# Kernel optimization log

Measured on AMD Instinct MI355X. Metric: run time of the kernel, lower is better.

Reference implementation:

```python
import jax, jax.numpy as jnp
import numpy as np

B, N, D, H, F = 2, 2048, 1024, 16, 4096
E = D // H
EPS = 1e-5

def layer_norm(x, g, b):
    mu = jnp.mean(x, axis=-1, keepdims=True)
    var = jnp.var(x, axis=-1, keepdims=True)
    return (x - mu) * jax.lax.rsqrt(var + EPS) * g + b

def setup_inputs() -> dict:
    key = jax.random.key(0)
    ks = jax.random.split(key, 16)
    s = lambda k, sh, fan: jax.random.normal(k, sh, jnp.float32) * (1.0 / np.sqrt(fan))
    return {
        'x': jax.random.normal(ks[0], (B, N, D), jnp.float32),
        'wq': s(ks[1], (D, D), D), 'bq': jnp.zeros((D,), jnp.float32),
        'wk': s(ks[2], (D, D), D), 'bk': jnp.zeros((D,), jnp.float32),
        'wv': s(ks[3], (D, D), D), 'bv': jnp.zeros((D,), jnp.float32),
        'w1': s(ks[4], (F, D), D), 'b1': jnp.zeros((F,), jnp.float32),
        'ln_mlp_g': jnp.ones((F,), jnp.float32), 'ln_mlp_b': jnp.zeros((F,), jnp.float32),
        'w2': s(ks[5], (D, F), F), 'b2': jnp.zeros((D,), jnp.float32),
        'ln1_g': jnp.ones((D,), jnp.float32), 'ln1_b': jnp.zeros((D,), jnp.float32),
        'ln2_g': jnp.ones((D,), jnp.float32), 'ln2_b': jnp.zeros((D,), jnp.float32),
    }

def reference(x, wq, bq, wk, bk, wv, bv, w1, b1, ln_mlp_g, ln_mlp_b, w2, b2, ln1_g, ln1_b, ln2_g, ln2_b):
    h = layer_norm(x, ln1_g, ln1_b)                       # [B,N,D]
    q = (h @ wq.T + bq).reshape(B, N, H, E).transpose(0, 2, 1, 3)  # [B,H,N,E]
    k = (h @ wk.T + bk).reshape(B, N, H, E).transpose(0, 2, 1, 3)
    v = (h @ wv.T + bv).reshape(B, N, H, E).transpose(0, 2, 1, 3)
    # faithful to source: score = q@k^T / sqrt(1/emb_dim) == q@k^T * sqrt(emb_dim)
    score = jnp.einsum('bhne,bhme->bhnm', q, k) * np.sqrt(D).astype(np.float32)
    causal = jnp.tril(jnp.ones((N, N), bool))
    score = jnp.where(causal[None, None], score, -jnp.inf)
    weight = jax.nn.softmax(score, axis=-1)
    attn = jnp.einsum('bhnm,bhme->bhne', weight, v)       # [B,H,N,E]
    attn = attn.transpose(0, 2, 1, 3).reshape(B, N, D)
    x = x + attn
    h2 = layer_norm(x, ln2_g, ln2_b)
    m = h2 @ w1.T + b1                                    # [B,N,F]
    m = jax.nn.relu(layer_norm(m, ln_mlp_g, ln_mlp_b))
    # faithful: no second residual in the source forward
    return m @ w2.T + b2
```

## Files before the change

### kernel.cpp

```cpp
#include <hip/hip_runtime.h>
#include <cstdint>

typedef __bf16 bf16_t;
typedef bf16_t bf16x8 __attribute__((ext_vector_type(8)));
typedef bf16_t bf16x4 __attribute__((ext_vector_type(4)));
typedef float  floatx4 __attribute__((ext_vector_type(4)));

#define GLD_LDS(g, l) __builtin_amdgcn_global_load_lds( \
    (const __attribute__((address_space(1))) unsigned int*)(g), \
    (__attribute__((address_space(3))) unsigned int*)(l), 16, 0, 0)

#define MFMA_BF16_16x16x32 __builtin_amdgcn_mfma_f32_16x16x32_bf16

__global__ __launch_bounds__(256) void prep(
    const float* __restrict__ wq, const float* __restrict__ wk,
    const float* __restrict__ wv, const float* __restrict__ w1,
    const float* __restrict__ w2, const float* __restrict__ bq,
    const float* __restrict__ bk,
    bf16_t* __restrict__ wqk_hi, bf16_t* __restrict__ wqk_lo,
    bf16_t* __restrict__ wvb, bf16_t* __restrict__ w1b, bf16_t* __restrict__ w2b,
    float* __restrict__ bqk) {
  const int blk = blockIdx.x, tid = threadIdx.x;
  if (blk < 2048) {
    const int qk = blk >> 10;
    const int i  = (blk & 1023) * 256 + tid;
    const float* src = qk ? wk : wq;
    float4 v = ((const float4*)src)[i];
    float f[4] = {v.x, v.y, v.z, v.w};
    bf16x4 h, l;
    #pragma unroll
    for (int j = 0; j < 4; ++j) { h[j] = (bf16_t)f[j]; l[j] = (bf16_t)(f[j] - (float)h[j]); }
    ((bf16x4*)(wqk_hi + qk * 1024 * 1024))[i] = h;
    ((bf16x4*)(wqk_lo + qk * 1024 * 1024))[i] = l;
  } else if (blk < 3072) {
    const int i = (blk - 2048) * 256 + tid;
    float4 v = ((const float4*)wv)[i];
    bf16x4 o; o[0]=(bf16_t)v.x; o[1]=(bf16_t)v.y; o[2]=(bf16_t)v.z; o[3]=(bf16_t)v.w;
    ((bf16x4*)wvb)[i] = o;
  } else if (blk < 7168) {
    const int i = (blk - 3072) * 256 + tid;
    float4 v = ((const float4*)w1)[i];
    bf16x4 o; o[0]=(bf16_t)v.x; o[1]=(bf16_t)v.y; o[2]=(bf16_t)v.z; o[3]=(bf16_t)v.w;
    ((bf16x4*)w1b)[i] = o;
  } else if (blk < 11264) {
    const int i = (blk - 7168) * 256 + tid;
    float4 v = ((const float4*)w2)[i];
    bf16x4 o; o[0]=(bf16_t)v.x; o[1]=(bf16_t)v.y; o[2]=(bf16_t)v.z; o[3]=(bf16_t)v.w;
    ((bf16x4*)w2b)[i] = o;
  } else {
    const int i = (blk - 11264) * 256 + tid;
    if (i < 1024) { bqk[i] = bq[i]; bqk[1024 + i] = bk[i]; }
  }
}


__device__ __forceinline__ void block_sum2(float& s, float& ss, float* red) {
  #pragma unroll
  for (int off = 32; off > 0; off >>= 1) {
    s  += __shfl_down(s, off);
    ss += __shfl_down(ss, off);
  }
  const int wave = threadIdx.x >> 6;
  if ((threadIdx.x & 63) == 0) { red[wave * 2] = s; red[wave * 2 + 1] = ss; }
  __syncthreads();
  s  = red[0] + red[2] + red[4] + red[6];
  ss = red[1] + red[3] + red[5] + red[7];
}

__global__ __launch_bounds__(256) void ln_fwd_split(const float* __restrict__ x,
    const float* __restrict__ g, const float* __restrict__ b,
    bf16_t* __restrict__ out_hi, bf16_t* __restrict__ out_lo) {
  __shared__ float red[8];
  const size_t row = blockIdx.x;
  float4 v = ((const float4*)(x + row * 1024))[threadIdx.x];
  float s  = v.x + v.y + v.z + v.w;
  float ss = v.x*v.x + v.y*v.y + v.z*v.z + v.w*v.w;
  block_sum2(s, ss, red);
  const float mu  = s * (1.f / 1024.f);
  const float var = ss * (1.f / 1024.f) - mu * mu;
  const float rs  = rsqrtf(var + 1e-5f);
  float4 gg = ((const float4*)g)[threadIdx.x];
  float4 bb = ((const float4*)b)[threadIdx.x];
  float f[4];
  f[0] = (v.x - mu) * rs * gg.x + bb.x;
  f[1] = (v.y - mu) * rs * gg.y + bb.y;
  f[2] = (v.z - mu) * rs * gg.z + bb.z;
  f[3] = (v.w - mu) * rs * gg.w + bb.w;
  bf16x4 oh, ol;
  #pragma unroll
  for (int j = 0; j < 4; ++j) {
    oh[j] = (bf16_t)f[j];
    ol[j] = (bf16_t)(f[j] - (float)oh[j]);
  }
  ((bf16x4*)(out_hi + row * 1024))[threadIdx.x] = oh;
  ((bf16x4*)(out_lo + row * 1024))[threadIdx.x] = ol;
}

__global__ __launch_bounds__(256) void resid_ln_fwd(const float* __restrict__ x,
    const float* __restrict__ a, const float* __restrict__ g, const float* __restrict__ b,
    bf16_t* __restrict__ out) {
  __shared__ float red[8];
  const size_t row = blockIdx.x;
  float4 v = ((const float4*)(x + row * 1024))[threadIdx.x];
  float4 av = ((const float4*)(a + row * 1024))[threadIdx.x];
  v.x += av.x; v.y += av.y; v.z += av.z; v.w += av.w;
  float s  = v.x + v.y + v.z + v.w;
  float ss = v.x*v.x + v.y*v.y + v.z*v.z + v.w*v.w;
  block_sum2(s, ss, red);
  const float mu  = s * (1.f / 1024.f);
  const float var = ss * (1.f / 1024.f) - mu * mu;
  const float rs  = rsqrtf(var + 1e-5f);
  float4 gg = ((const float4*)g)[threadIdx.x];
  float4 bb = ((const float4*)b)[threadIdx.x];
  bf16x4 o;
  o[0] = (bf16_t)((v.x - mu) * rs * gg.x + bb.x);
  o[1] = (bf16_t)((v.y - mu) * rs * gg.y + bb.y);
  o[2] = (bf16_t)((v.z - mu) * rs * gg.z + bb.z);
  o[3] = (bf16_t)((v.w - mu) * rs * gg.w + bb.w);
  ((bf16x4*)(out + row * 1024))[threadIdx.x] = o;
}

__global__ __launch_bounds__(256) void ln_relu_inplace(bf16_t* __restrict__ m,
    const float* __restrict__ g, const float* __restrict__ b) {
  __shared__ float red[8];
  const size_t row = blockIdx.x;
  bf16_t* mr = m + row * 4096;
  const int base = threadIdx.x * 16;
  bf16x8 v0 = *(bf16x8*)(mr + base);
  bf16x8 v1 = *(bf16x8*)(mr + base + 8);
  float f[16];
  #pragma unroll
  for (int i = 0; i < 8; ++i) { f[i] = (float)v0[i]; f[8 + i] = (float)v1[i]; }
  float s = 0.f, ss = 0.f;
  #pragma unroll
  for (int i = 0; i < 16; ++i) { s += f[i]; ss += f[i] * f[i]; }
  block_sum2(s, ss, red);
  const float mu  = s * (1.f / 4096.f);
  const float var = ss * (1.f / 4096.f) - mu * mu;
  const float rs  = rsqrtf(var + 1e-5f);
  bf16x8 o0, o1;
  #pragma unroll
  for (int i = 0; i < 16; ++i) {
    float ov = (f[i] - mu) * rs * g[base + i] + b[base + i];
    ov = fmaxf(ov, 0.f);
    if (i < 8) o0[i] = (bf16_t)ov; else o1[i - 8] = (bf16_t)ov;
  }
  *(bf16x8*)(mr + base) = o0;
  *(bf16x8*)(mr + base + 8) = o1;
}

__device__ __forceinline__ void xcd_swizzle(int& bx, int& by) {
  const int gx = gridDim.x;
  const int nwg = gx * gridDim.y;
  const int flat = by * gx + bx;
  const int cpx = nwg >> 3;
  const int swz = (flat & 7) * cpx + (flat >> 3);
  bx = swz % gx; by = swz / gx;
}

template <int OUT_MODE, int BM>
__global__ __launch_bounds__(256) void gemm_bt(
    const bf16_t* __restrict__ A, const bf16_t* __restrict__ Bw,
    const float* __restrict__ bias, void* __restrict__ Cp,
    int M, int N, int K) {
  constexpr int MI = BM / 32;
  __shared__ bf16_t As[BM * 32];
  __shared__ bf16_t Bs[128 * 32];
  const int tid  = threadIdx.x;
  const int wave = tid >> 6, lane = tid & 63;
  const int quad = lane >> 4, l15 = lane & 15;
  int bx = blockIdx.x, by = blockIdx.y;
  xcd_swizzle(bx, by);
  const int m0 = bx * BM, n0 = by * 128;
  const int wm = (wave >> 1) * (BM / 2), wn = (wave & 1) * 64;
  const int srowA = wave * (BM / 4) + (lane >> 2);
  const int srowB = wave * 32 + (lane >> 2);
  const int scol = (lane & 3) * 8;

  floatx4 acc[MI][4] = {};

  const bf16_t* Ag = A  + (size_t)(m0 + srowA) * K + scol;
  const bf16_t* Bg = Bw + (size_t)(n0 + srowB) * K + scol;

  for (int k0 = 0; k0 < K; k0 += 32) {
    __syncthreads();
    #pragma unroll
    for (int i = 0; i < BM / 64; ++i)
      GLD_LDS(Ag + (size_t)(i * 16) * K + k0, As + wave * (BM / 4) * 32 + i * 512);
    #pragma unroll
    for (int i = 0; i < 2; ++i)
      GLD_LDS(Bg + (size_t)(i * 16) * K + k0, Bs + wave * 1024 + i * 512);
    __syncthreads();
    bf16x8 af[MI], bfr[4];
    #pragma unroll
    for (int i = 0; i < MI; ++i)
      af[i] = *(const bf16x8*)(As + (wm + i * 16 + l15) * 32 + quad * 8);
    #pragma unroll
    for (int j = 0; j < 4; ++j)
      bfr[j] = *(const bf16x8*)(Bs + (wn + j * 16 + l15) * 32 + quad * 8);
    #pragma unroll
    for (int i = 0; i < MI; ++i)
      #pragma unroll
      for (int j = 0; j < 4; ++j)
        acc[i][j] = MFMA_BF16_16x16x32(af[i], bfr[j], acc[i][j], 0, 0, 0);
  }
  #pragma unroll
  for (int j = 0; j < 4; ++j) {
    const int col = n0 + wn + j * 16 + l15;
    const float bv = bias[col];
    #pragma unroll
    for (int i = 0; i < MI; ++i) {
      #pragma unroll
      for (int r = 0; r < 4; ++r) {
        const int row = m0 + wm + i * 16 + quad * 4 + r;
        const float v = acc[i][j][r] + bv;
        if (OUT_MODE == 0) {
          ((float*)Cp)[(size_t)row * N + col] = v;
        } else if (OUT_MODE == 1) {
          ((bf16_t*)Cp)[(size_t)row * N + col] = (bf16_t)v;
        } else {
          const int b = row >> 11, n = row & 2047;
          const int h = col >> 6, e = col & 63;
          ((bf16_t*)Cp)[(((size_t)((b << 4) + h) * 2048 + n) << 6) + e] = (bf16_t)v;
        }
      }
    }
  }
}

__global__ __launch_bounds__(256) void gemm_qk_split(
    const bf16_t* __restrict__ Ah, const bf16_t* __restrict__ Al,
    const bf16_t* __restrict__ Bh, const bf16_t* __restrict__ Bl,
    const float* __restrict__ bias,
    bf16_t* __restrict__ qhi, bf16_t* __restrict__ qlo,
    bf16_t* __restrict__ khi, bf16_t* __restrict__ klo,
    int M, int N, int K) {
  __shared__ bf16_t Ash[64 * 32];
  __shared__ bf16_t Asl[64 * 32];
  __shared__ bf16_t Bsh[128 * 32];
  __shared__ bf16_t Bsl[128 * 32];
  const int tid  = threadIdx.x;
  const int wave = tid >> 6, lane = tid & 63;
  const int quad = lane >> 4, l15 = lane & 15;
  int bx = blockIdx.x, by = blockIdx.y;
  xcd_swizzle(bx, by);
  const int m0 = bx * 64, n0 = by * 128;
  const int wm = (wave >> 1) * 32, wn = (wave & 1) * 64;
  const int srowA = wave * 16 + (lane >> 2);
  const int srowB = wave * 32 + (lane >> 2);
  const int scol = (lane & 3) * 8;

  floatx4 acc[2][4] = {};

  const size_t aoff = (size_t)(m0 + srowA) * K + scol;
  const size_t boff = (size_t)(n0 + srowB) * K + scol;

  for (int k0 = 0; k0 < K; k0 += 32) {
    __syncthreads();
    GLD_LDS(Ah + aoff + k0, Ash + wave * 512);
    GLD_LDS(Al + aoff + k0, Asl + wave * 512);
    #pragma unroll
    for (int i = 0; i < 2; ++i) {
      const size_t gb = boff + (size_t)(i * 16) * K + k0;
      GLD_LDS(Bh + gb, Bsh + wave * 1024 + i * 512);
      GLD_LDS(Bl + gb, Bsl + wave * 1024 + i * 512);
    }
    __syncthreads();
    bf16x8 ah[2], al[2], bh[4], bl[4];
    #pragma unroll
    for (int i = 0; i < 2; ++i) {
      const int ro = (wm + i * 16 + l15) * 32 + quad * 8;
      ah[i] = *(const bf16x8*)(Ash + ro);
      al[i] = *(const bf16x8*)(Asl + ro);
    }
    #pragma unroll
    for (int j = 0; j < 4; ++j) {
      const int ro = (wn + j * 16 + l15) * 32 + quad * 8;
      bh[j] = *(const bf16x8*)(Bsh + ro);
      bl[j] = *(const bf16x8*)(Bsl + ro);
    }
    #pragma unroll
    for (int i = 0; i < 2; ++i)
      #pragma unroll
      for (int j = 0; j < 4; ++j) {
        acc[i][j] = MFMA_BF16_16x16x32(ah[i], bh[j], acc[i][j], 0, 0, 0);
        acc[i][j] = MFMA_BF16_16x16x32(ah[i], bl[j], acc[i][j], 0, 0, 0);
        acc[i][j] = MFMA_BF16_16x16x32(al[i], bh[j], acc[i][j], 0, 0, 0);
      }
  }
  #pragma unroll
  for (int j = 0; j < 4; ++j) {
    const int col = n0 + wn + j * 16 + l15;
    const float bv = bias[col];
    const bool isq = col < 1024;
    bf16_t* hib = isq ? qhi : khi;
    bf16_t* lob = isq ? qlo : klo;
    const float scale = isq ? 32.0f : 1.0f;
    const int h = (col >> 6) & 15, e = col & 63;
    #pragma unroll
    for (int i = 0; i < 2; ++i) {
      #pragma unroll
      for (int r = 0; r < 4; ++r) {
        const int row = m0 + wm + i * 16 + quad * 4 + r;
        const int b = row >> 11, n = row & 2047;
        const float c = (acc[i][j][r] + bv) * scale;
        const bf16_t chi = (bf16_t)c;
        const bf16_t clo = (bf16_t)(c - (float)chi);
        const size_t dst = (((size_t)((b << 4) + h) * 2048 + n) << 6) + e;
        hib[dst] = chi;
        lob[dst] = clo;
      }
    }
  }
}

__global__ __launch_bounds__(256) void transpose_v(
    const bf16_t* __restrict__ vhm, bf16_t* __restrict__ vT) {
  __shared__ bf16_t T[64 * 72];
  const int bh = blockIdx.x, n0 = blockIdx.y * 64;
  const int r = threadIdx.x >> 2;
  const int c = (threadIdx.x & 3) * 16;
  const bf16_t* src = vhm + ((size_t)bh * 2048 + n0 + r) * 64 + c;
  bf16x8 a0 = *(const bf16x8*)src;
  bf16x8 a1 = *(const bf16x8*)(src + 8);
  #pragma unroll
  for (int j = 0; j < 8; ++j) {
    T[(c + j) * 72 + r]     = a0[j];
    T[(c + 8 + j) * 72 + r] = a1[j];
  }
  __syncthreads();
  bf16x8 o0 = *(const bf16x8*)(T + r * 72 + c);
  bf16x8 o1 = *(const bf16x8*)(T + r * 72 + c + 8);
  bf16_t* dst = vT + ((size_t)(bh * 64 + r)) * 2048 + n0 + c;
  *(bf16x8*)dst = o0;
  *(bf16x8*)(dst + 8) = o1;
}

#define SWZ(row, chunk) (((row) << 6) + ((((chunk) ^ ((row) & 7))) << 3))
__global__ __launch_bounds__(256, 4) void attn_causal(
    const bf16_t* __restrict__ qhi, const bf16_t* __restrict__ qlo,
    const bf16_t* __restrict__ khi, const bf16_t* __restrict__ klo,
    const bf16_t* __restrict__ vT, float* __restrict__ o) {
  __shared__ bf16_t KsH[64 * 64];
  __shared__ bf16_t KsL[64 * 64];
  __shared__ bf16_t Vt[64 * 64];
  __shared__ bf16_t Ps[4][16 * 64];

  const int tid  = threadIdx.x;
  const int wave = tid >> 6, lane = tid & 63;
  const int quad = lane >> 4, l15 = lane & 15;
  const int bh = blockIdx.x;
  const int q0 = (31 - (int)blockIdx.y) * 64;
  const size_t hb = (size_t)bh * 2048;

  const int wmin = q0 + wave * 16;
  const int qrow = wmin + l15;
  bf16x8 qh[2], ql[2];
  {
    const bf16_t* qbh = qhi + ((hb + wmin + l15) << 6) + quad * 8;
    const bf16_t* qbl = qlo + ((hb + wmin + l15) << 6) + quad * 8;
    qh[0] = *(const bf16x8*)qbh;
    qh[1] = *(const bf16x8*)(qbh + 32);
    ql[0] = *(const bf16x8*)qbl;
    ql[1] = *(const bf16x8*)(qbl + 32);
  }

  floatx4 accO[4] = {};
  float m_row = -1e30f;
  float l_row = 0.f;

  const int kr = wave * 16 + (lane >> 3);
  const int kc7 = lane & 7;
  const bf16_t* kgh = khi + ((hb + kr) << 6) + kc7 * 8;
  const bf16_t* kgl = klo + ((hb + kr) << 6) + kc7 * 8;
  const bf16_t* vg  = vT + ((size_t)(bh * 64 + kr)) * 2048 + kc7 * 8;

  bf16x8 pkh0 = *(const bf16x8*)(kgh);
  bf16x8 pkh1 = *(const bf16x8*)(kgh + (8 << 6));
  bf16x8 pkl0 = *(const bf16x8*)(kgl);
  bf16x8 pkl1 = *(const bf16x8*)(kgl + (8 << 6));
  bf16x8 pv0  = *(const bf16x8*)(vg);
  bf16x8 pv1  = *(const bf16x8*)(vg + 8 * 2048);

  const int ntiles = (q0 >> 6) + 1;
  for (int t = 0; t < ntiles; ++t) {
    const int k0 = t * 64;
    __syncthreads();
    *(bf16x8*)(KsH + SWZ(kr, kc7))     = pkh0;
    *(bf16x8*)(KsH + SWZ(kr + 8, kc7)) = pkh1;
    *(bf16x8*)(KsL + SWZ(kr, kc7))     = pkl0;
    *(bf16x8*)(KsL + SWZ(kr + 8, kc7)) = pkl1;
    *(bf16x8*)(Vt  + SWZ(kr, kc7))     = pv0;
    *(bf16x8*)(Vt  + SWZ(kr + 8, kc7)) = pv1;
    if (t + 1 < ntiles) {
      const int koff = (t + 1) << 12;
      pkh0 = *(const bf16x8*)(kgh + koff);
      pkh1 = *(const bf16x8*)(kgh + koff + (8 << 6));
      pkl0 = *(const bf16x8*)(kgl + koff);
      pkl1 = *(const bf16x8*)(kgl + koff + (8 << 6));
      pv0  = *(const bf16x8*)(vg + (t + 1) * 64);
      pv1  = *(const bf16x8*)(vg + (t + 1) * 64 + 8 * 2048);
    }
    __syncthreads();

    const bool needmask = (k0 + 63 > wmin);

    floatx4 sv[4];
    __builtin_amdgcn_s_setprio(1);
    #pragma unroll
    for (int j = 0; j < 4; ++j) {
      const int rK = j * 16 + l15;
      const bf16x8 kh0 = *(const bf16x8*)(KsH + SWZ(rK, quad));
      const bf16x8 kh1 = *(const bf16x8*)(KsH + SWZ(rK, quad + 4));
      const bf16x8 kl0 = *(const bf16x8*)(KsL + SWZ(rK, quad));
      const bf16x8 kl1 = *(const bf16x8*)(KsL + SWZ(rK, quad + 4));
      floatx4 acc = {};
      acc = MFMA_BF16_16x16x32(kh0, qh[0], acc, 0, 0, 0);
      acc = MFMA_BF16_16x16x32(kh1, qh[1], acc, 0, 0, 0);
      acc = MFMA_BF16_16x16x32(kl0, qh[0], acc, 0, 0, 0);
      acc = MFMA_BF16_16x16x32(kl1, qh[1], acc, 0, 0, 0);
      acc = MFMA_BF16_16x16x32(kh0, ql[0], acc, 0, 0, 0);
      acc = MFMA_BF16_16x16x32(kh1, ql[1], acc, 0, 0, 0);
      sv[j] = acc;
    }
    __builtin_amdgcn_s_setprio(0);

    const int lim = qrow - k0 - quad * 4;
    float mr = -1e30f;
    #pragma unroll
    for (int j = 0; j < 4; ++j)
      #pragma unroll
      for (int r = 0; r < 4; ++r) {
        float x = sv[j][r];
        if (needmask && (j * 16 + r > lim)) x = -1e30f;
        sv[j][r] = x;
        mr = fmaxf(mr, x);
      }
    mr = fmaxf(mr, __shfl_xor(mr, 16));
    mr = fmaxf(mr, __shfl_xor(mr, 32));
    const float mold = m_row;
    const float mnew = fmaxf(mold, mr);
    m_row = mnew;
    float psum = 0.f;
    bf16x4 pb[4];
    #pragma unroll
    for (int j = 0; j < 4; ++j)
      #pragma unroll
      for (int r = 0; r < 4; ++r) {
        const float p = __expf(sv[j][r] - mnew);
        const bf16_t pv = (bf16_t)p;
        psum += (float)pv;
        pb[j][r] = pv;
      }
    {
      bf16_t* pw = &Ps[wave][0];
      #pragma unroll
      for (int j = 0; j < 4; ++j)
        *(bf16x4*)(pw + SWZ(l15, 2 * j + (quad >> 1)) + (quad & 1) * 4) = pb[j];
    }
    psum += __shfl_xor(psum, 16);
    psum += __shfl_xor(psum, 32);
    const float alpha = __expf(mold - mnew);
    l_row = l_row * alpha + psum;
    if (__any(mnew > mold)) {
      #pragma unroll
      for (int r = 0; r < 4; ++r) {
        const float ar = __shfl(alpha, quad * 4 + r);
        #pragma unroll
        for (int j = 0; j < 4; ++j) accO[j][r] *= ar;
      }
    }
    asm volatile("s_waitcnt lgkmcnt(0)" ::: "memory");
    __builtin_amdgcn_sched_barrier(0);

    bf16x8 pf[2];
    {
      const bf16_t* pw = &Ps[wave][0];
      pf[0] = *(const bf16x8*)(pw + SWZ(l15, quad));
      pf[1] = *(const bf16x8*)(pw + SWZ(l15, quad + 4));
    }
    __builtin_amdgcn_s_setprio(1);
    #pragma unroll
    for (int j = 0; j < 4; ++j) {
      const int rV = j * 16 + l15;
      const bf16x8 vf0 = *(const bf16x8*)(Vt + SWZ(rV, quad));
      const bf16x8 vf1 = *(const bf16x8*)(Vt + SWZ(rV, quad + 4));
      accO[j] = MFMA_BF16_16x16x32(pf[0], vf0, accO[j], 0, 0, 0);
      accO[j] = MFMA_BF16_16x16x32(pf[1], vf1, accO[j], 0, 0, 0);
    }
    __builtin_amdgcn_s_setprio(0);
  }

  const int b = bh >> 4, h = bh & 15;
  #pragma unroll
  for (int r = 0; r < 4; ++r) {
    const float lr = __shfl(l_row, quad * 4 + r);
    const float linv = 1.f / lr;
    const int qr = wmin + quad * 4 + r;
    float* orow = o + ((size_t)(b * 2048) + qr) * 1024 + h * 64;
    #pragma unroll
    for (int j = 0; j < 4; ++j)
      orow[j * 16 + l15] = accO[j][r] * linv;
  }
}


extern "C" void kernel_launch(void* const* d_in, const int* in_sizes, int n_in,
                              void* d_out, int out_size, void* d_ws, size_t ws_size,
                              hipStream_t stream) {
  const float* x        = (const float*)d_in[0];
  const float* wq       = (const float*)d_in[1];
  const float* bq       = (const float*)d_in[2];
  const float* wk       = (const float*)d_in[3];
  const float* bk       = (const float*)d_in[4];
  const float* wv       = (const float*)d_in[5];
  const float* bv       = (const float*)d_in[6];
  const float* w1       = (const float*)d_in[7];
  const float* b1       = (const float*)d_in[8];
  const float* ln_mlp_g = (const float*)d_in[9];
  const float* ln_mlp_b = (const float*)d_in[10];
  const float* w2       = (const float*)d_in[11];
  const float* b2       = (const float*)d_in[12];
  const float* ln1_g    = (const float*)d_in[13];
  const float* ln1_b    = (const float*)d_in[14];
  const float* ln2_g    = (const float*)d_in[15];
  const float* ln2_b    = (const float*)d_in[16];

  char* ws = (char*)d_ws;
  bf16_t* h_hi   = (bf16_t*)(ws);
  bf16_t* h_lo   = (bf16_t*)(ws + (8u  << 20));
  bf16_t* vTb    = (bf16_t*)(ws);
  bf16_t* wqk_hi = (bf16_t*)(ws + (16u << 20));
  bf16_t* wqk_lo = (bf16_t*)(ws + (20u << 20));
  bf16_t* wvb    = (bf16_t*)(ws + (24u << 20));
  float*  bqk    = (float*) (ws + (26u << 20));
  bf16_t* w1b    = (bf16_t*)(ws + (28u << 20));
  bf16_t* w2b    = (bf16_t*)(ws + (36u << 20));
  bf16_t* qhi    = (bf16_t*)(ws + (44u << 20));
  bf16_t* qlo    = (bf16_t*)(ws + (52u << 20));
  bf16_t* khi    = (bf16_t*)(ws + (60u << 20));
  bf16_t* klo    = (bf16_t*)(ws + (68u << 20));
  bf16_t* mbuf   = (bf16_t*)(ws + (44u << 20));
  bf16_t* vhm    = (bf16_t*)(ws + (76u << 20));
  float*  attnb  = (float*) (ws + (84u << 20));
  bf16_t* h2     = (bf16_t*)(ws + (100u << 20));

  prep<<<11268, 256, 0, stream>>>(wq, wk, wv, w1, w2, bq, bk,
                                  wqk_hi, wqk_lo, wvb, w1b, w2b, bqk);

  ln_fwd_split<<<4096, 256, 0, stream>>>(x, ln1_g, ln1_b, h_hi, h_lo);
  gemm_qk_split<<<dim3(64, 16), 256, 0, stream>>>(h_hi, h_lo, wqk_hi, wqk_lo, bqk,
                                                  qhi, qlo, khi, klo, 4096, 2048, 1024);
  gemm_bt<2, 64><<<dim3(64, 8), 256, 0, stream>>>(h_hi, wvb, bv, vhm, 4096, 1024, 1024);
  transpose_v<<<dim3(32, 32), 256, 0, stream>>>(vhm, vTb);
  attn_causal<<<dim3(32, 32), 256, 0, stream>>>(qhi, qlo, khi, klo, vTb, attnb);
  resid_ln_fwd<<<4096, 256, 0, stream>>>(x, attnb, ln2_g, ln2_b, h2);
  gemm_bt<1, 128><<<dim3(32, 32), 256, 0, stream>>>(h2, w1b, b1, mbuf, 4096, 4096, 1024);
  ln_relu_inplace<<<4096, 256, 0, stream>>>(mbuf, ln_mlp_g, ln_mlp_b);
  gemm_bt<0, 64><<<dim3(64, 8), 256, 0, stream>>>(mbuf, w2b, b2, d_out, 4096, 1024, 4096);

  (void)in_sizes; (void)n_in; (void)out_size; (void)ws_size;
}
```

Baseline: 443.2 us.

## Split-K the final MLP GEMM with atomics and change XCD block mapping

The final down-projection GEMM (K=4096) is split into two K halves across a new grid z dimension. Partial results are accumulated into the output with float atomicAdd, and the output is zeroed by a memset first; only the first split adds the bias. This doubles the number of workgroups for a GEMM that otherwise launches only 512 blocks. The XCD swizzle is also replaced by a chunked 2D mapping that gives each XCD a contiguous band of M-tiles, which changes L2 locality for all GEMMs. The cost is atomic traffic, an extra memset launch, and non-deterministic summation order.

After: 445.7 us. About the same (+0.6%).

```diff
diff --git a/kernel.cpp b/kernel.cpp
--- a/kernel.cpp
+++ b/kernel.cpp
@@ -149,16 +149,17 @@
   *(bf16x8*)(mr + base + 8) = o1;
 }
 
-__device__ __forceinline__ void xcd_swizzle(int& bx, int& by) {
+__device__ __forceinline__ void xcd_chunk2d(int& bx, int& by) {
   const int gx = gridDim.x;
-  const int nwg = gx * gridDim.y;
-  const int flat = by * gx + bx;
-  const int cpx = nwg >> 3;
-  const int swz = (flat & 7) * cpx + (flat >> 3);
-  bx = swz % gx; by = swz / gx;
-}
-
-template <int OUT_MODE, int BM>
+  const int f  = (int)(blockIdx.y * gx + blockIdx.x);
+  const int xcd = f & 7;
+  const int i = f >> 3;
+  const int bxPer = gx >> 3;
+  by = i / bxPer;
+  bx = xcd * bxPer + (i - by * bxPer);
+}
+
+template <int OUT_MODE, int BM, int SK>
 __global__ __launch_bounds__(256) void gemm_bt(
     const bf16_t* __restrict__ A, const bf16_t* __restrict__ Bw,
     const float* __restrict__ bias, void* __restrict__ Cp,
@@ -170,19 +171,21 @@
   const int wave = tid >> 6, lane = tid & 63;
   const int quad = lane >> 4, l15 = lane & 15;
   int bx = blockIdx.x, by = blockIdx.y;
-  xcd_swizzle(bx, by);
+  xcd_chunk2d(bx, by);
   const int m0 = bx * BM, n0 = by * 128;
   const int wm = (wave >> 1) * (BM / 2), wn = (wave & 1) * 64;
   const int srowA = wave * (BM / 4) + (lane >> 2);
   const int srowB = wave * 32 + (lane >> 2);
   const int scol = (lane & 3) * 8;
+  const int ks = (SK > 1) ? (int)blockIdx.z : 0;
+  const int kbeg = ks * (K / SK), kend = kbeg + K / SK;
 
   floatx4 acc[MI][4] = {};
 
   const bf16_t* Ag = A  + (size_t)(m0 + srowA) * K + scol;
   const bf16_t* Bg = Bw + (size_t)(n0 + srowB) * K + scol;
 
-  for (int k0 = 0; k0 < K; k0 += 32) {
+  for (int k0 = kbeg; k0 < kend; k0 += 32) {
     __syncthreads();
     #pragma unroll
     for (int i = 0; i < BM / 64; ++i)
@@ -207,7 +210,7 @@
   #pragma unroll
   for (int j = 0; j < 4; ++j) {
     const int col = n0 + wn + j * 16 + l15;
-    const float bv = bias[col];
+    const float bv = (SK == 1 || ks == 0) ? bias[col] : 0.f;
     #pragma unroll
     for (int i = 0; i < MI; ++i) {
       #pragma unroll
@@ -215,7 +218,8 @@
         const int row = m0 + wm + i * 16 + quad * 4 + r;
         const float v = acc[i][j][r] + bv;
         if (OUT_MODE == 0) {
-          ((float*)Cp)[(size_t)row * N + col] = v;
+          if (SK > 1) atomicAdd(&((float*)Cp)[(size_t)row * N + col], v);
+          else        ((float*)Cp)[(size_t)row * N + col] = v;
         } else if (OUT_MODE == 1) {
           ((bf16_t*)Cp)[(size_t)row * N + col] = (bf16_t)v;
         } else {
@@ -243,7 +247,7 @@
   const int wave = tid >> 6, lane = tid & 63;
   const int quad = lane >> 4, l15 = lane & 15;
   int bx = blockIdx.x, by = blockIdx.y;
-  xcd_swizzle(bx, by);
+  xcd_chunk2d(bx, by);
   const int m0 = bx * 64, n0 = by * 128;
   const int wm = (wave >> 1) * 32, wn = (wave & 1) * 64;
   const int srowA = wave * 16 + (lane >> 2);
@@ -545,19 +549,21 @@
   float*  attnb  = (float*) (ws + (84u << 20));
   bf16_t* h2     = (bf16_t*)(ws + (100u << 20));
 
+  hipMemsetAsync(d_out, 0, (size_t)4096 * 1024 * sizeof(float), stream);
+
   prep<<<11268, 256, 0, stream>>>(wq, wk, wv, w1, w2, bq, bk,
                                   wqk_hi, wqk_lo, wvb, w1b, w2b, bqk);
 
   ln_fwd_split<<<4096, 256, 0, stream>>>(x, ln1_g, ln1_b, h_hi, h_lo);
   gemm_qk_split<<<dim3(64, 16), 256, 0, stream>>>(h_hi, h_lo, wqk_hi, wqk_lo, bqk,
                                                   qhi, qlo, khi, klo, 4096, 2048, 1024);
-  gemm_bt<2, 64><<<dim3(64, 8), 256, 0, stream>>>(h_hi, wvb, bv, vhm, 4096, 1024, 1024);
+  gemm_bt<2, 64, 1><<<dim3(64, 8), 256, 0, stream>>>(h_hi, wvb, bv, vhm, 4096, 1024, 1024);
   transpose_v<<<dim3(32, 32), 256, 0, stream>>>(vhm, vTb);
   attn_causal<<<dim3(32, 32), 256, 0, stream>>>(qhi, qlo, khi, klo, vTb, attnb);
   resid_ln_fwd<<<4096, 256, 0, stream>>>(x, attnb, ln2_g, ln2_b, h2);
-  gemm_bt<1, 128><<<dim3(32, 32), 256, 0, stream>>>(h2, w1b, b1, mbuf, 4096, 4096, 1024);
+  gemm_bt<1, 128, 1><<<dim3(32, 32), 256, 0, stream>>>(h2, w1b, b1, mbuf, 4096, 4096, 1024);
   ln_relu_inplace<<<4096, 256, 0, stream>>>(mbuf, ln_mlp_g, ln_mlp_b);
-  gemm_bt<0, 64><<<dim3(64, 8), 256, 0, stream>>>(mbuf, w2b, b2, d_out, 4096, 1024, 4096);
+  gemm_bt<0, 64, 2><<<dim3(64, 8, 2), 256, 0, stream>>>(mbuf, w2b, b2, d_out, 4096, 1024, 4096);
 
   (void)in_sizes; (void)n_in; (void)out_size; (void)ws_size;
 }
```
